# Kernel tuning notes

Hardware: AMD Instinct MI355X
Metric: run time of the kernel (lower is better)

## Reference

```python
import jax, jax.numpy as jnp
import numpy as np

KERNELS = (5, 13, 25)


def _moving_avg(x, k):
    # x: [B, L, C]; replicate-pad by (k-1)//2 on each side of time dim, then mean-pool window k, stride 1.
    p = (k - 1) // 2
    front = jnp.repeat(x[:, :1, :], p, axis=1)
    end = jnp.repeat(x[:, -1:, :], p, axis=1)
    xp = jnp.concatenate([front, x, end], axis=1)  # [B, L+2p, C]
    cs = jnp.cumsum(xp, axis=1)
    cs = jnp.concatenate([jnp.zeros_like(cs[:, :1, :]), cs], axis=1)  # prepend zero row
    return (cs[:, k:, :] - cs[:, :-k, :]) / k  # [B, L, C] (odd k)


def _circular_conv(x, w):
    # x: [B, Cin, T], w: [Cout, Cin, 3]; circular padding of 1 on each side (padding_mode='circular', padding=1)
    xp = jnp.concatenate([x[:, :, -1:], x, x[:, :, :1]], axis=2)
    return jax.lax.conv_general_dilated(xp, w, window_strides=(1,), padding='VALID',
                                        dimension_numbers=('NCH', 'OIH', 'NCH'))


def setup_inputs() -> dict:
    key = jax.random.key(0)
    k0, k1, k2, k3 = jax.random.split(key, 4)
    B, L, C = 64, 96, 2048  # L must equal c_in=96 (conv applied without permute)
    x = jax.random.normal(k0, (B, L, C), dtype=jnp.float32)
    conv_w = jax.random.normal(k1, (96, 96, 3), dtype=jnp.float32) * (1.0 / np.sqrt(96 * 3))
    gate_w = jax.random.normal(k2, (len(KERNELS), 1), dtype=jnp.float32)
    gate_b = jax.random.normal(k3, (len(KERNELS),), dtype=jnp.float32)
    return {"x": x, "conv_w": conv_w, "gate_w": gate_w, "gate_b": gate_b}


def reference(x, conv_w, gate_w, gate_b):
    # multi-scale moving averages stacked on last axis: [B, L, C, K]
    means = jnp.stack([_moving_avg(x, k) for k in KERNELS], axis=-1)
    # gate: Linear(1, K) on x.unsqueeze(-1), softmax over K
    logits = x[..., None] * gate_w[:, 0] + gate_b  # [B, L, C, K]
    gate = jax.nn.softmax(logits, axis=-1)
    moving_mean = jnp.sum(means * gate, axis=-1)  # [B, L, C]
    res = x - moving_mean
    # conv treats dim 1 (L=96) as channels, dim 2 (C) as spatial length — as in the torch code
    return (_circular_conv(res, conv_w), _circular_conv(moving_mean, conv_w))
```

## Files before the change

kernel.cpp:

```cpp
#include <hip/hip_runtime.h>
#include <hip/hip_bf16.h>

typedef __attribute__((ext_vector_type(8))) short short8;
typedef __attribute__((ext_vector_type(8))) unsigned short u16x8;
typedef __attribute__((ext_vector_type(4))) unsigned short u16x4;
typedef __attribute__((ext_vector_type(4))) float f32x4;

constexpr int NB = 64;
constexpr int NL = 96;
constexpr int NC = 2048;
constexpr int TT = 64;
constexpr int KTOT = 288;
constexpr int LROW = 104;
constexpr float LOG2E = 1.44269504088896340736f;

__device__ inline unsigned short f2bf(float f) {
    union { float f; unsigned u; } v; v.f = f;
    unsigned r = v.u + 0x7fff + ((v.u >> 16) & 1);
    return (unsigned short)(r >> 16);
}
__device__ inline unsigned cvt_pk_bf16(float lo, float hi) {
    unsigned r;
    asm("v_cvt_pk_bf16_f32 %0, %1, %2" : "=v"(r) : "v"(lo), "v"(hi));
    return r;
}
__device__ inline float fexp2(float x) {
    float r; asm("v_exp_f32 %0, %1" : "=v"(r) : "v"(x)); return r;
}
__device__ inline float frcp(float x) {
    float r; asm("v_rcp_f32 %0, %1" : "=v"(r) : "v"(x)); return r;
}
__device__ inline float bflo(unsigned d) { return __uint_as_float(d << 16); }
__device__ inline float bfhi(unsigned d) { return __uint_as_float(d & 0xffff0000u); }

__global__ void prep_aw(const float* __restrict__ w, unsigned short* __restrict__ aw)
{
    int idx = blockIdx.x * 256 + threadIdx.x;
    if (idx >= NL * KTOT) return;
    int o = idx / KTOT, k = idx - o * KTOT;
    int tau = k / NL, i = k - tau * NL;
    aw[idx] = f2bf(w[(o * NL + i) * 3 + tau]);
}

template<int Q>
__device__ __forceinline__ void winq(
    const unsigned* __restrict__ srow,
    unsigned short* __restrict__ mrow,
    float w0, float w1, float w2, float b0, float b1, float b2)
{
    constexpr int L0 = Q * 24;
    constexpr int DW0 = (Q == 0) ? 0 : 12 * Q - 6;
    constexpr int NDW = (Q == 0 || Q == 3) ? 18 : 24;

    unsigned dv[NDW];
#pragma unroll
    for (int d = 0; d < NDW; ++d) dv[d] = srow[DW0 + d];

#define CLMP(r) ((r) < 0 ? 0 : ((r) > 95 ? 95 : (r)))
#define VAL(r) ((CLMP(r) & 1) ? bfhi(dv[(CLMP(r) >> 1) - DW0]) \
                              : bflo(dv[(CLMP(r) >> 1) - DW0]))

    float s5 = 0.0f, s13 = 0.0f, s25 = 0.0f;
#pragma unroll
    for (int d = -12; d <= 12; ++d) {
        float v = VAL(L0 + d);
        s25 += v;
        if (d >= -6 && d <= 6) s13 += v;
        if (d >= -2 && d <= 2) s5 += v;
    }

    unsigned md[12];
    float pm = 0.0f;
#pragma unroll
    for (int i = 0; i < 24; ++i) {
        const int l = L0 + i;
        if (i > 0) {
            s25 += VAL(l + 12) - VAL(l - 13);
            s13 += VAL(l + 6)  - VAL(l - 7);
            s5  += VAL(l + 2)  - VAL(l - 3);
        }
        float xl = VAL(l);
        float e0 = fexp2(fmaf(xl, w0, b0));
        float e1 = fexp2(fmaf(xl, w1, b1));
        float e2 = fexp2(fmaf(xl, w2, b2));
        float inv = frcp(e0 + e1 + e2);
        float mmv = fmaf(s5 * 0.2f, e0,
                    fmaf(s13 * (1.0f / 13.0f), e1,
                         s25 * 0.04f * e2)) * inv;
        if ((i & 1) == 0) pm = mmv;
        else              md[i >> 1] = cvt_pk_bf16(pm, mmv);
    }
#undef VAL
#undef CLMP

#pragma unroll
    for (int v = 0; v < 6; ++v) {
        union { u16x4 vv; unsigned d[2]; } o;
        o.d[0] = md[2 * v]; o.d[1] = md[2 * v + 1];
        *(u16x4*)(mrow + L0 + 4 * v) = o.vv;
    }
}

__global__ __launch_bounds__(256, 4) void fused3(
    const float* __restrict__ x,
    const float* __restrict__ gw,
    const float* __restrict__ gb,
    const unsigned short* __restrict__ aw,
    float* __restrict__ out0,
    float* __restrict__ out1)
{
    __shared__ __align__(16) unsigned short sx[2][TT + 2][LROW];

    int b = blockIdx.x;
    int t0 = blockIdx.y * TT;
    size_t xb = (size_t)b * NL * NC;

    int lane = threadIdx.x & 63;
    int wv = threadIdx.x >> 6;
    int lr = lane & 15, lk = lane >> 4;

    for (int u = threadIdx.x; u < 768; u += 256) {
        int l2 = u >> 4, cq = u & 15;
        const float* p0 = x + xb + (size_t)(2 * l2) * NC + t0 + 4 * cq;
        f32x4 a = *(const f32x4*)p0;
        f32x4 bv = *(const f32x4*)(p0 + NC);
#pragma unroll
        for (int j = 0; j < 4; ++j)
            *(unsigned*)(&sx[0][1 + 4 * cq + j][2 * l2]) = cvt_pk_bf16(a[j], bv[j]);
    }
    if (threadIdx.x < 96) {
        int u = threadIdx.x;
        int e = u / 48, l2 = u - e * 48;
        int t = e ? ((t0 + TT) & (NC - 1)) : ((t0 - 1) & (NC - 1));
        int c = e ? 65 : 0;
        const float* p0 = x + xb + (size_t)(2 * l2) * NC + t;
        *(unsigned*)(&sx[0][c][2 * l2]) = cvt_pk_bf16(p0[0], p0[NC]);
    }
    __syncthreads();

    {
        float w0 = gw[0] * LOG2E, w1 = gw[1] * LOG2E, w2 = gw[2] * LOG2E;
        float b0 = gb[0] * LOG2E, b1 = gb[1] * LOG2E, b2 = gb[2] * LOG2E;

        {
            const unsigned* srow = (const unsigned*)&sx[0][lane][0];
            unsigned short* mrow = &sx[1][lane][0];
            if (wv == 0)      winq<0>(srow, mrow, w0, w1, w2, b0, b1, b2);
            else if (wv == 1) winq<1>(srow, mrow, w0, w1, w2, b0, b1, b2);
            else if (wv == 2) winq<2>(srow, mrow, w0, w1, w2, b0, b1, b2);
            else              winq<3>(srow, mrow, w0, w1, w2, b0, b1, b2);
        }
        if (threadIdx.x < 192) {
            int ce = 64 + (threadIdx.x & 1);
            int l  = threadIdx.x >> 1;
            const unsigned short* col = &sx[0][ce][0];
            float s5 = 0.0f, s13 = 0.0f, s25 = 0.0f;
#pragma unroll
            for (int d = -12; d <= 12; ++d) {
                int li = l + d; li = li < 0 ? 0 : (li > 95 ? 95 : li);
                float v = __uint_as_float(((unsigned)col[li]) << 16);
                s25 += v;
                if (d >= -6 && d <= 6) s13 += v;
                if (d >= -2 && d <= 2) s5 += v;
            }
            float xl = __uint_as_float(((unsigned)col[l]) << 16);
            float e0 = fexp2(fmaf(xl, w0, b0));
            float e1 = fexp2(fmaf(xl, w1, b1));
            float e2 = fexp2(fmaf(xl, w2, b2));
            float inv = frcp(e0 + e1 + e2);
            float mmv = fmaf(s5 * 0.2f, e0,
                        fmaf(s13 * (1.0f / 13.0f), e1,
                             s25 * 0.04f * e2)) * inv;
            sx[1][ce][l] = (unsigned short)(cvt_pk_bf16(mmv, mmv) & 0xffffu);
        }
    }

    int mg = wv & 1, ng = wv >> 1;
    const unsigned short* abase = aw + (size_t)(mg * 48 + lr) * KTOT + lk * 8;
    short8 aCur[3], aNxt[3];
#pragma unroll
    for (int mt = 0; mt < 3; ++mt)
        aCur[mt] = *(const short8*)(abase + mt * 16 * KTOT);

    __syncthreads();

    f32x4 acc[3][2][2] = {};

#pragma unroll
    for (int ks = 0; ks < 9; ++ks) {
        if (ks < 8) {
#pragma unroll
            for (int mt = 0; mt < 3; ++mt)
                aNxt[mt] = *(const short8*)(abase + mt * 16 * KTOT + (ks + 1) * 32);
        }
        const int tau = ks / 3;
        const int i0 = (ks - tau * 3) * 32;
        short8 bfx[2], bfm[2];
#pragma unroll
        for (int nt = 0; nt < 2; ++nt) {
            int r = ng * 32 + nt * 16 + lr + tau;
            bfx[nt] = *(const short8*)(&sx[0][r][i0 + lk * 8]);
            bfm[nt] = *(const short8*)(&sx[1][r][i0 + lk * 8]);
        }
#pragma unroll
        for (int mt = 0; mt < 3; ++mt)
#pragma unroll
            for (int nt = 0; nt < 2; ++nt) {
                acc[mt][nt][0] = __builtin_amdgcn_mfma_f32_16x16x32_bf16(
                    aCur[mt], bfx[nt], acc[mt][nt][0], 0, 0, 0);
                acc[mt][nt][1] = __builtin_amdgcn_mfma_f32_16x16x32_bf16(
                    aCur[mt], bfm[nt], acc[mt][nt][1], 0, 0, 0);
            }
#pragma unroll
        for (int mt = 0; mt < 3; ++mt) aCur[mt] = aNxt[mt];
    }

    int tw = t0 + ng * 32 + lr;
#pragma unroll
    for (int mt = 0; mt < 3; ++mt) {
        int o0 = mg * 48 + mt * 16 + lk * 4;
#pragma unroll
        for (int nt = 0; nt < 2; ++nt) {
#pragma unroll
            for (int r4 = 0; r4 < 4; ++r4) {
                size_t idx = xb + (size_t)(o0 + r4) * NC + tw + nt * 16;
                float vm = acc[mt][nt][1][r4];
                out1[idx] = vm;
                out0[idx] = acc[mt][nt][0][r4] - vm;
            }
        }
    }
}

extern "C" void kernel_launch(void* const* d_in, const int* in_sizes, int n_in,
                              void* d_out, int out_size, void* d_ws, size_t ws_size,
                              hipStream_t stream)
{
    const float* x      = (const float*)d_in[0];
    const float* conv_w = (const float*)d_in[1];
    const float* gate_w = (const float*)d_in[2];
    const float* gate_b = (const float*)d_in[3];

    float* out0 = (float*)d_out;
    float* out1 = out0 + (size_t)NB * NL * NC;

    unsigned short* awb = (unsigned short*)d_ws;

    prep_aw<<<dim3((NL * KTOT + 255) / 256), 256, 0, stream>>>(conv_w, awb);
    fused3<<<dim3(NB, NC / TT), 256, 0, stream>>>(x, gate_w, gate_b, awb, out0, out1);
}
```

Before: 44.10 us.

## Split conv GEMM into x-pass before barrier and mean-pass after, pack gate math

The conv MFMA loop is split in two. The GEMM over the raw-x tile runs right after the moving-average computation without waiting for the second barrier, and the GEMM over the moving-mean tile runs after the barrier. This lets one wave's x-GEMM overlap other waves' gate and window work, which is meant to hide the sync stall. Gate logits and two window sums are also packed into float2 ops to invite packed FP32 instructions, and launch bounds are raised to 5 blocks per SM. The cost is reloading the A fragments for the second pass and possible register pressure from the higher occupancy target.

```diff
diff --git a/kernel.cpp b/kernel.cpp
--- a/kernel.cpp
+++ b/kernel.cpp
@@ -5,6 +5,7 @@
 typedef __attribute__((ext_vector_type(8))) unsigned short u16x8;
 typedef __attribute__((ext_vector_type(4))) unsigned short u16x4;
 typedef __attribute__((ext_vector_type(4))) float f32x4;
+typedef __attribute__((ext_vector_type(2))) float f32x2;
 
 constexpr int NB = 64;
 constexpr int NL = 96;
@@ -46,7 +47,7 @@
 __device__ __forceinline__ void winq(
     const unsigned* __restrict__ srow,
     unsigned short* __restrict__ mrow,
-    float w0, float w1, float w2, float b0, float b1, float b2)
+    f32x2 w01, f32x2 b01, float w2, float b2)
 {
     constexpr int L0 = Q * 24;
     constexpr int DW0 = (Q == 0) ? 0 : 12 * Q - 6;
@@ -60,14 +61,15 @@
 #define VAL(r) ((CLMP(r) & 1) ? bfhi(dv[(CLMP(r) >> 1) - DW0]) \
                               : bflo(dv[(CLMP(r) >> 1) - DW0]))
 
-    float s5 = 0.0f, s13 = 0.0f, s25 = 0.0f;
+    float s5i = 0.0f, s13i = 0.0f, s25 = 0.0f;
 #pragma unroll
     for (int d = -12; d <= 12; ++d) {
         float v = VAL(L0 + d);
         s25 += v;
-        if (d >= -6 && d <= 6) s13 += v;
-        if (d >= -2 && d <= 2) s5 += v;
-    }
+        if (d >= -6 && d <= 6) s13i += v;
+        if (d >= -2 && d <= 2) s5i += v;
+    }
+    f32x2 s513 = {s5i, s13i};
 
     unsigned md[12];
     float pm = 0.0f;
@@ -76,16 +78,17 @@
         const int l = L0 + i;
         if (i > 0) {
             s25 += VAL(l + 12) - VAL(l - 13);
-            s13 += VAL(l + 6)  - VAL(l - 7);
-            s5  += VAL(l + 2)  - VAL(l - 3);
+            s513 += (f32x2){VAL(l + 2), VAL(l + 6)};
+            s513 -= (f32x2){VAL(l - 3), VAL(l - 7)};
         }
         float xl = VAL(l);
-        float e0 = fexp2(fmaf(xl, w0, b0));
-        float e1 = fexp2(fmaf(xl, w1, b1));
+        f32x2 lg = (f32x2){xl, xl} * w01 + b01;
+        float e0 = fexp2(lg.x);
+        float e1 = fexp2(lg.y);
         float e2 = fexp2(fmaf(xl, w2, b2));
         float inv = frcp(e0 + e1 + e2);
-        float mmv = fmaf(s5 * 0.2f, e0,
-                    fmaf(s13 * (1.0f / 13.0f), e1,
+        float mmv = fmaf(s513.x * 0.2f, e0,
+                    fmaf(s513.y * (1.0f / 13.0f), e1,
                          s25 * 0.04f * e2)) * inv;
         if ((i & 1) == 0) pm = mmv;
         else              md[i >> 1] = cvt_pk_bf16(pm, mmv);
@@ -101,7 +104,7 @@
     }
 }
 
-__global__ __launch_bounds__(256, 4) void fused3(
+__global__ __launch_bounds__(256, 5) void fused4(
     const float* __restrict__ x,
     const float* __restrict__ gw,
     const float* __restrict__ gb,
@@ -139,16 +142,17 @@
     __syncthreads();
 
     {
-        float w0 = gw[0] * LOG2E, w1 = gw[1] * LOG2E, w2 = gw[2] * LOG2E;
-        float b0 = gb[0] * LOG2E, b1 = gb[1] * LOG2E, b2 = gb[2] * LOG2E;
+        f32x2 w01 = {gw[0] * LOG2E, gw[1] * LOG2E};
+        f32x2 b01 = {gb[0] * LOG2E, gb[1] * LOG2E};
+        float w2 = gw[2] * LOG2E, b2 = gb[2] * LOG2E;
 
         {
             const unsigned* srow = (const unsigned*)&sx[0][lane][0];
             unsigned short* mrow = &sx[1][lane][0];
-            if (wv == 0)      winq<0>(srow, mrow, w0, w1, w2, b0, b1, b2);
-            else if (wv == 1) winq<1>(srow, mrow, w0, w1, w2, b0, b1, b2);
-            else if (wv == 2) winq<2>(srow, mrow, w0, w1, w2, b0, b1, b2);
-            else              winq<3>(srow, mrow, w0, w1, w2, b0, b1, b2);
+            if (wv == 0)      winq<0>(srow, mrow, w01, b01, w2, b2);
+            else if (wv == 1) winq<1>(srow, mrow, w01, b01, w2, b2);
+            else if (wv == 2) winq<2>(srow, mrow, w01, b01, w2, b2);
+            else              winq<3>(srow, mrow, w01, b01, w2, b2);
         }
         if (threadIdx.x < 192) {
             int ce = 64 + (threadIdx.x & 1);
@@ -164,8 +168,8 @@
                 if (d >= -2 && d <= 2) s5 += v;
             }
             float xl = __uint_as_float(((unsigned)col[l]) << 16);
-            float e0 = fexp2(fmaf(xl, w0, b0));
-            float e1 = fexp2(fmaf(xl, w1, b1));
+            float e0 = fexp2(fmaf(xl, w01.x, b01.x));
+            float e1 = fexp2(fmaf(xl, w01.y, b01.y));
             float e2 = fexp2(fmaf(xl, w2, b2));
             float inv = frcp(e0 + e1 + e2);
             float mmv = fmaf(s5 * 0.2f, e0,
@@ -182,9 +186,7 @@
     for (int mt = 0; mt < 3; ++mt)
         aCur[mt] = *(const short8*)(abase + mt * 16 * KTOT);
 
-    __syncthreads();
-
-    f32x4 acc[3][2][2] = {};
+    f32x4 accx[3][2] = {}, accm[3][2] = {};
 
 #pragma unroll
     for (int ks = 0; ks < 9; ++ks) {
@@ -195,22 +197,49 @@
         }
         const int tau = ks / 3;
         const int i0 = (ks - tau * 3) * 32;
-        short8 bfx[2], bfm[2];
+        short8 bfx[2];
 #pragma unroll
         for (int nt = 0; nt < 2; ++nt) {
             int r = ng * 32 + nt * 16 + lr + tau;
             bfx[nt] = *(const short8*)(&sx[0][r][i0 + lk * 8]);
+        }
+#pragma unroll
+        for (int mt = 0; mt < 3; ++mt)
+#pragma unroll
+            for (int nt = 0; nt < 2; ++nt)
+                accx[mt][nt] = __builtin_amdgcn_mfma_f32_16x16x32_bf16(
+                    aCur[mt], bfx[nt], accx[mt][nt], 0, 0, 0);
+#pragma unroll
+        for (int mt = 0; mt < 3; ++mt) aCur[mt] = aNxt[mt];
+    }
+
+#pragma unroll
+    for (int mt = 0; mt < 3; ++mt)
+        aCur[mt] = *(const short8*)(abase + mt * 16 * KTOT);
+
+    __syncthreads();
+
+#pragma unroll
+    for (int ks = 0; ks < 9; ++ks) {
+        if (ks < 8) {
+#pragma unroll
+            for (int mt = 0; mt < 3; ++mt)
+                aNxt[mt] = *(const short8*)(abase + mt * 16 * KTOT + (ks + 1) * 32);
+        }
+        const int tau = ks / 3;
+        const int i0 = (ks - tau * 3) * 32;
+        short8 bfm[2];
+#pragma unroll
+        for (int nt = 0; nt < 2; ++nt) {
+            int r = ng * 32 + nt * 16 + lr + tau;
             bfm[nt] = *(const short8*)(&sx[1][r][i0 + lk * 8]);
         }
 #pragma unroll
         for (int mt = 0; mt < 3; ++mt)
 #pragma unroll
-            for (int nt = 0; nt < 2; ++nt) {
-                acc[mt][nt][0] = __builtin_amdgcn_mfma_f32_16x16x32_bf16(
-                    aCur[mt], bfx[nt], acc[mt][nt][0], 0, 0, 0);
-                acc[mt][nt][1] = __builtin_amdgcn_mfma_f32_16x16x32_bf16(
-                    aCur[mt], bfm[nt], acc[mt][nt][1], 0, 0, 0);
-            }
+            for (int nt = 0; nt < 2; ++nt)
+                accm[mt][nt] = __builtin_amdgcn_mfma_f32_16x16x32_bf16(
+                    aCur[mt], bfm[nt], accm[mt][nt], 0, 0, 0);
 #pragma unroll
         for (int mt = 0; mt < 3; ++mt) aCur[mt] = aNxt[mt];
     }
@@ -224,9 +253,9 @@
 #pragma unroll
             for (int r4 = 0; r4 < 4; ++r4) {
                 size_t idx = xb + (size_t)(o0 + r4) * NC + tw + nt * 16;
-                float vm = acc[mt][nt][1][r4];
+                float vm = accm[mt][nt][r4];
                 out1[idx] = vm;
-                out0[idx] = acc[mt][nt][0][r4] - vm;
+                out0[idx] = accx[mt][nt][r4] - vm;
             }
         }
     }
@@ -247,5 +276,5 @@
     unsigned short* awb = (unsigned short*)d_ws;
 
     prep_aw<<<dim3((NL * KTOT + 255) / 256), 256, 0, stream>>>(conv_w, awb);
-    fused3<<<dim3(NB, NC / TT), 256, 0, stream>>>(x, gate_w, gate_b, awb, out0, out1);
-}
+    fused4<<<dim3(NB, NC / TT), 256, 0, stream>>>(x, gate_w, gate_b, awb, out0, out1);
+}
```

New measurement: 55.23 us. +25.2%, slower.

## Make fused kernel persistent with double-buffered tile prefetch across tiles

Applied to the files above, without the earlier changes.

Replaces the one-tile-per-block grid (2048 blocks) with 768 blocks, each processing 2 or 3 consecutive tiles. The next tile's global loads are issued into registers before the current tile's moving-average and MFMA work, then written to a second LDS buffer, so load latency overlaps compute. This also drops the launch-bounds occupancy hint. The costs are more registers held for prefetch, a third LDS buffer, and uneven per-block work (3 vs 2 tiles) that may leave a tail.

```diff
diff --git a/kernel.cpp b/kernel.cpp
--- a/kernel.cpp
+++ b/kernel.cpp
@@ -12,6 +12,7 @@
 constexpr int TT = 64;
 constexpr int KTOT = 288;
 constexpr int LROW = 104;
+constexpr int NTILE = 2048;
 constexpr float LOG2E = 1.44269504088896340736f;
 
 __device__ inline unsigned short f2bf(float f) {
@@ -101,7 +102,7 @@
     }
 }
 
-__global__ __launch_bounds__(256, 4) void fused3(
+__global__ __launch_bounds__(256) void fused6(
     const float* __restrict__ x,
     const float* __restrict__ gw,
     const float* __restrict__ gb,
@@ -109,127 +110,175 @@
     float* __restrict__ out0,
     float* __restrict__ out1)
 {
-    __shared__ __align__(16) unsigned short sx[2][TT + 2][LROW];
-
-    int b = blockIdx.x;
-    int t0 = blockIdx.y * TT;
-    size_t xb = (size_t)b * NL * NC;
-
-    int lane = threadIdx.x & 63;
-    int wv = threadIdx.x >> 6;
-    int lr = lane & 15, lk = lane >> 4;
-
-    for (int u = threadIdx.x; u < 768; u += 256) {
-        int l2 = u >> 4, cq = u & 15;
-        const float* p0 = x + xb + (size_t)(2 * l2) * NC + t0 + 4 * cq;
-        f32x4 a = *(const f32x4*)p0;
-        f32x4 bv = *(const f32x4*)(p0 + NC);
-#pragma unroll
-        for (int j = 0; j < 4; ++j)
-            *(unsigned*)(&sx[0][1 + 4 * cq + j][2 * l2]) = cvt_pk_bf16(a[j], bv[j]);
-    }
-    if (threadIdx.x < 96) {
-        int u = threadIdx.x;
-        int e = u / 48, l2 = u - e * 48;
-        int t = e ? ((t0 + TT) & (NC - 1)) : ((t0 - 1) & (NC - 1));
-        int c = e ? 65 : 0;
-        const float* p0 = x + xb + (size_t)(2 * l2) * NC + t;
-        *(unsigned*)(&sx[0][c][2 * l2]) = cvt_pk_bf16(p0[0], p0[NC]);
-    }
+    __shared__ __align__(16) unsigned short sxA[TT + 2][LROW];
+    __shared__ __align__(16) unsigned short sxB[TT + 2][LROW];
+    __shared__ __align__(16) unsigned short sm[TT + 2][LROW];
+
+    const int tid = threadIdx.x;
+    const int lane = tid & 63;
+    const int wv = tid >> 6;
+    const int lr = lane & 15, lk = lane >> 4;
+    const int mg = wv & 1, ng = wv >> 1;
+
+    int blk = blockIdx.x;
+    int tlo, thi;
+    if (blk < 512) { tlo = 3 * blk;              thi = tlo + 3; }
+    else           { tlo = 1536 + 2 * (blk - 512); thi = tlo + 2; }
+
+    const float w0 = gw[0] * LOG2E, w1 = gw[1] * LOG2E, w2 = gw[2] * LOG2E;
+    const float b0 = gb[0] * LOG2E, b1 = gb[1] * LOG2E, b2 = gb[2] * LOG2E;
+
+    f32x4 fa[3], fb[3];
+    float ea = 0.0f, eb = 0.0f;
+
+#define STAGE_ISSUE(TILE) do {                                               \
+        int b_ = (TILE) >> 5;                                                \
+        int t0_ = ((TILE) & 31) * TT;                                        \
+        const float* xb_ = x + (size_t)b_ * NL * NC;                         \
+        _Pragma("unroll")                                                    \
+        for (int it = 0; it < 3; ++it) {                                     \
+            int u = tid + it * 256;                                          \
+            int l2 = u >> 4, cq = u & 15;                                    \
+            const float* p0 = xb_ + (size_t)(2 * l2) * NC + t0_ + 4 * cq;    \
+            fa[it] = *(const f32x4*)p0;                                      \
+            fb[it] = *(const f32x4*)(p0 + NC);                               \
+        }                                                                    \
+        if (tid < 96) {                                                      \
+            int e_ = tid / 48, l2 = tid - e_ * 48;                           \
+            int t_ = e_ ? ((t0_ + TT) & (NC - 1)) : ((t0_ - 1) & (NC - 1));  \
+            const float* p0 = xb_ + (size_t)(2 * l2) * NC + t_;              \
+            ea = p0[0]; eb = p0[NC];                                         \
+        }                                                                    \
+    } while (0)
+
+#define STAGE_WRITE(DST) do {                                                \
+        _Pragma("unroll")                                                    \
+        for (int it = 0; it < 3; ++it) {                                     \
+            int u = tid + it * 256;                                          \
+            int l2 = u >> 4, cq = u & 15;                                    \
+            _Pragma("unroll")                                                \
+            for (int j = 0; j < 4; ++j)                                      \
+                *(unsigned*)(&(DST)[1 + 4 * cq + j][2 * l2]) =               \
+                    cvt_pk_bf16(fa[it][j], fb[it][j]);                       \
+        }                                                                    \
+        if (tid < 96) {                                                      \
+            int e_ = tid / 48, l2 = tid - e_ * 48;                           \
+            int c_ = e_ ? 65 : 0;                                            \
+            *(unsigned*)(&(DST)[c_][2 * l2]) = cvt_pk_bf16(ea, eb);          \
+        }                                                                    \
+    } while (0)
+
+    STAGE_ISSUE(tlo);
+    STAGE_WRITE(sxA);
     __syncthreads();
 
-    {
-        float w0 = gw[0] * LOG2E, w1 = gw[1] * LOG2E, w2 = gw[2] * LOG2E;
-        float b0 = gb[0] * LOG2E, b1 = gb[1] * LOG2E, b2 = gb[2] * LOG2E;
+    int cur = 0;
+    for (int t = tlo; t < thi; ++t) {
+        unsigned short (*xc)[LROW] = cur ? sxB : sxA;
+        unsigned short (*xn)[LROW] = cur ? sxA : sxB;
+        const bool more = (t + 1 < thi);
+
+        if (more) STAGE_ISSUE(t + 1);
 
         {
-            const unsigned* srow = (const unsigned*)&sx[0][lane][0];
-            unsigned short* mrow = &sx[1][lane][0];
+            const unsigned* srow = (const unsigned*)&xc[lane][0];
+            unsigned short* mrow = &sm[lane][0];
             if (wv == 0)      winq<0>(srow, mrow, w0, w1, w2, b0, b1, b2);
             else if (wv == 1) winq<1>(srow, mrow, w0, w1, w2, b0, b1, b2);
             else if (wv == 2) winq<2>(srow, mrow, w0, w1, w2, b0, b1, b2);
             else              winq<3>(srow, mrow, w0, w1, w2, b0, b1, b2);
-        }
-        if (threadIdx.x < 192) {
-            int ce = 64 + (threadIdx.x & 1);
-            int l  = threadIdx.x >> 1;
-            const unsigned short* col = &sx[0][ce][0];
-            float s5 = 0.0f, s13 = 0.0f, s25 = 0.0f;
-#pragma unroll
-            for (int d = -12; d <= 12; ++d) {
-                int li = l + d; li = li < 0 ? 0 : (li > 95 ? 95 : li);
-                float v = __uint_as_float(((unsigned)col[li]) << 16);
-                s25 += v;
-                if (d >= -6 && d <= 6) s13 += v;
-                if (d >= -2 && d <= 2) s5 += v;
-            }
-            float xl = __uint_as_float(((unsigned)col[l]) << 16);
-            float e0 = fexp2(fmaf(xl, w0, b0));
-            float e1 = fexp2(fmaf(xl, w1, b1));
-            float e2 = fexp2(fmaf(xl, w2, b2));
-            float inv = frcp(e0 + e1 + e2);
-            float mmv = fmaf(s5 * 0.2f, e0,
-                        fmaf(s13 * (1.0f / 13.0f), e1,
-                             s25 * 0.04f * e2)) * inv;
-            sx[1][ce][l] = (unsigned short)(cvt_pk_bf16(mmv, mmv) & 0xffffu);
-        }
-    }
-
-    int mg = wv & 1, ng = wv >> 1;
-    const unsigned short* abase = aw + (size_t)(mg * 48 + lr) * KTOT + lk * 8;
-    short8 aCur[3], aNxt[3];
-#pragma unroll
-    for (int mt = 0; mt < 3; ++mt)
-        aCur[mt] = *(const short8*)(abase + mt * 16 * KTOT);
-
-    __syncthreads();
-
-    f32x4 acc[3][2][2] = {};
-
-#pragma unroll
-    for (int ks = 0; ks < 9; ++ks) {
-        if (ks < 8) {
-#pragma unroll
-            for (int mt = 0; mt < 3; ++mt)
-                aNxt[mt] = *(const short8*)(abase + mt * 16 * KTOT + (ks + 1) * 32);
-        }
-        const int tau = ks / 3;
-        const int i0 = (ks - tau * 3) * 32;
-        short8 bfx[2], bfm[2];
-#pragma unroll
-        for (int nt = 0; nt < 2; ++nt) {
-            int r = ng * 32 + nt * 16 + lr + tau;
-            bfx[nt] = *(const short8*)(&sx[0][r][i0 + lk * 8]);
-            bfm[nt] = *(const short8*)(&sx[1][r][i0 + lk * 8]);
-        }
-#pragma unroll
-        for (int mt = 0; mt < 3; ++mt)
-#pragma unroll
-            for (int nt = 0; nt < 2; ++nt) {
-                acc[mt][nt][0] = __builtin_amdgcn_mfma_f32_16x16x32_bf16(
-                    aCur[mt], bfx[nt], acc[mt][nt][0], 0, 0, 0);
-                acc[mt][nt][1] = __builtin_amdgcn_mfma_f32_16x16x32_bf16(
-                    aCur[mt], bfm[nt], acc[mt][nt][1], 0, 0, 0);
-            }
-#pragma unroll
-        for (int mt = 0; mt < 3; ++mt) aCur[mt] = aNxt[mt];
-    }
-
-    int tw = t0 + ng * 32 + lr;
-#pragma unroll
-    for (int mt = 0; mt < 3; ++mt) {
-        int o0 = mg * 48 + mt * 16 + lk * 4;
-#pragma unroll
-        for (int nt = 0; nt < 2; ++nt) {
-#pragma unroll
-            for (int r4 = 0; r4 < 4; ++r4) {
-                size_t idx = xb + (size_t)(o0 + r4) * NC + tw + nt * 16;
-                float vm = acc[mt][nt][1][r4];
-                out1[idx] = vm;
-                out0[idx] = acc[mt][nt][0][r4] - vm;
+
+            if (tid < 192) {
+                int ce = 64 + (tid & 1);
+                int l  = tid >> 1;
+                const unsigned short* col = &xc[ce][0];
+                float s5 = 0.0f, s13 = 0.0f, s25 = 0.0f;
+#pragma unroll
+                for (int d = -12; d <= 12; ++d) {
+                    int li = l + d; li = li < 0 ? 0 : (li > 95 ? 95 : li);
+                    float v = __uint_as_float(((unsigned)col[li]) << 16);
+                    s25 += v;
+                    if (d >= -6 && d <= 6) s13 += v;
+                    if (d >= -2 && d <= 2) s5 += v;
+                }
+                float xl = __uint_as_float(((unsigned)col[l]) << 16);
+                float e0 = fexp2(fmaf(xl, w0, b0));
+                float e1 = fexp2(fmaf(xl, w1, b1));
+                float e2 = fexp2(fmaf(xl, w2, b2));
+                float inv = frcp(e0 + e1 + e2);
+                float mmv = fmaf(s5 * 0.2f, e0,
+                            fmaf(s13 * (1.0f / 13.0f), e1,
+                                 s25 * 0.04f * e2)) * inv;
+                sm[ce][l] = (unsigned short)(cvt_pk_bf16(mmv, mmv) & 0xffffu);
             }
         }
+
+        if (more) STAGE_WRITE(xn);
+
+        const unsigned short* abase = aw + (size_t)(mg * 48 + lr) * KTOT + lk * 8;
+        short8 aCur[3], aNxt[3];
+#pragma unroll
+        for (int mt = 0; mt < 3; ++mt)
+            aCur[mt] = *(const short8*)(abase + mt * 16 * KTOT);
+
+        __syncthreads();
+
+        f32x4 acc[3][2][2] = {};
+#pragma unroll
+        for (int ks = 0; ks < 9; ++ks) {
+            if (ks < 8) {
+#pragma unroll
+                for (int mt = 0; mt < 3; ++mt)
+                    aNxt[mt] = *(const short8*)(abase + mt * 16 * KTOT + (ks + 1) * 32);
+            }
+            const int tau = ks / 3;
+            const int i0 = (ks - tau * 3) * 32;
+            short8 bfx[2], bfm[2];
+#pragma unroll
+            for (int nt = 0; nt < 2; ++nt) {
+                int r = ng * 32 + nt * 16 + lr + tau;
+                bfx[nt] = *(const short8*)(&xc[r][i0 + lk * 8]);
+                bfm[nt] = *(const short8*)(&sm[r][i0 + lk * 8]);
+            }
+#pragma unroll
+            for (int mt = 0; mt < 3; ++mt)
+#pragma unroll
+                for (int nt = 0; nt < 2; ++nt) {
+                    acc[mt][nt][0] = __builtin_amdgcn_mfma_f32_16x16x32_bf16(
+                        aCur[mt], bfx[nt], acc[mt][nt][0], 0, 0, 0);
+                    acc[mt][nt][1] = __builtin_amdgcn_mfma_f32_16x16x32_bf16(
+                        aCur[mt], bfm[nt], acc[mt][nt][1], 0, 0, 0);
+                }
+#pragma unroll
+            for (int mt = 0; mt < 3; ++mt) aCur[mt] = aNxt[mt];
+        }
+
+        {
+            int bb = t >> 5;
+            int t0 = (t & 31) * TT;
+            size_t ob = (size_t)bb * NL * NC;
+            int tw = t0 + ng * 32 + lr;
+#pragma unroll
+            for (int mt = 0; mt < 3; ++mt) {
+                int o0 = mg * 48 + mt * 16 + lk * 4;
+#pragma unroll
+                for (int nt = 0; nt < 2; ++nt) {
+#pragma unroll
+                    for (int r4 = 0; r4 < 4; ++r4) {
+                        size_t idx = ob + (size_t)(o0 + r4) * NC + tw + nt * 16;
+                        float vm = acc[mt][nt][1][r4];
+                        out1[idx] = vm;
+                        out0[idx] = acc[mt][nt][0][r4] - vm;
+                    }
+                }
+            }
+        }
+
+        __syncthreads();
+        cur ^= 1;
     }
+#undef STAGE_ISSUE
+#undef STAGE_WRITE
 }
 
 extern "C" void kernel_launch(void* const* d_in, const int* in_sizes, int n_in,
@@ -247,5 +296,5 @@
     unsigned short* awb = (unsigned short*)d_ws;
 
     prep_aw<<<dim3((NL * KTOT + 255) / 256), 256, 0, stream>>>(conv_w, awb);
-    fused3<<<dim3(NB, NC / TT), 256, 0, stream>>>(x, gate_w, gate_b, awb, out0, out1);
-}
+    fused6<<<dim3(768), 256, 0, stream>>>(x, gate_w, gate_b, awb, out0, out1);
+}
```

After: 59.15 us. 34.1% more time.
